# Optimization experiments

Measured on AMD Instinct MI355X. Metric: run time of the kernel, lower is better.

## Reference

```python
import jax, jax.numpy as jnp
import numpy as np

N_NODES = 50000
N_EDGES = 600000
IN_DIM = 128
HID = 128
OUT_DIM = 10
N_GRAPHS = 512
LN_EPS = 1e-5
N_CELLS = 4  # len(macro_architecture) + 1


def setup_inputs() -> dict:
    key = jax.random.key(0)
    ks = jax.random.split(key, 8)
    s = 0.05
    x = jax.random.normal(ks[0], (N_NODES, IN_DIM), dtype=jnp.float32)
    edge_index = jax.random.randint(ks[1], (2, N_EDGES), 0, N_NODES, dtype=jnp.int32)
    batch = jnp.sort(jax.random.randint(ks[2], (N_NODES,), 0, N_GRAPHS, dtype=jnp.int32))
    return {
        "x": x,
        "edge_index": edge_index,
        "batch": batch,
        "W_pre": jax.random.normal(ks[3], (IN_DIM, HID), dtype=jnp.float32) * s,
        "b_pre": jnp.zeros((HID,), jnp.float32),
        "conv_W": jax.random.normal(ks[4], (N_CELLS, HID, HID), dtype=jnp.float32) * s,
        "conv_b": jnp.zeros((N_CELLS, HID), jnp.float32),
        "ln_g": jnp.ones((N_CELLS, HID), jnp.float32),
        "ln_b": jnp.zeros((N_CELLS, HID), jnp.float32),
        "W_post": jax.random.normal(ks[5], (HID, OUT_DIM), dtype=jnp.float32) * s,
        "b_post": jnp.zeros((OUT_DIM,), jnp.float32),
    }


def _gcn_conv(x, W, b, src, dst):
    """GCNConv: add self-loops, symmetric deg^-1/2 normalization, gather-scatter."""
    n = x.shape[0]
    h = x @ W                                   # [N, HID]
    loops = jnp.arange(n, dtype=src.dtype)
    s = jnp.concatenate([src, loops])           # [E + N]
    d = jnp.concatenate([dst, loops])
    deg = jax.ops.segment_sum(jnp.ones_like(d, jnp.float32), d, num_segments=n)
    dinv = jax.lax.rsqrt(jnp.maximum(deg, 1.0))  # deg >= 1 via self-loops
    coef = dinv[s] * dinv[d]                    # [E + N]
    out = jax.ops.segment_sum(h[s] * coef[:, None], d, num_segments=n)
    return out + b


def _layer_norm(x, g, b):
    mu = jnp.mean(x, axis=-1, keepdims=True)
    var = jnp.var(x, axis=-1, keepdims=True)
    return (x - mu) * jax.lax.rsqrt(var + LN_EPS) * g + b


def _cell(x, i, conv_W, conv_b, ln_g, ln_b, src, dst):
    h = _gcn_conv(x, conv_W[i], conv_b[i], src, dst)
    return jax.nn.relu(_layer_norm(h, ln_g[i], ln_b[i]))


def reference(x, edge_index, batch, W_pre, b_pre, conv_W, conv_b, ln_g, ln_b, W_post, b_post):
    src, dst = edge_index[0], edge_index[1]
    # pre MLP
    h0 = x @ W_pre + b_pre
    # state node 0 (all 3 outgoing edges active -> identical output reused)
    n0 = _cell(h0, 0, conv_W, conv_b, ln_g, ln_b, src, dst)
    # state node 1: input = node0's output
    n1 = _cell(n0, 1, conv_W, conv_b, ln_g, ln_b, src, dst)
    # second-to-last node: sum of [-2] outputs (n0, n1)
    s2l = _cell(n0 + n1, 2, conv_W, conv_b, ln_g, ln_b, src, dst)
    # last node: sum of [-1] outputs (n0, n1) + second-to-last output
    last = _cell(n0 + n1 + s2l, 3, conv_W, conv_b, ln_g, ln_b, src, dst)
    # sum pooling by graph id, then post MLP
    pooled = jax.ops.segment_sum(last, batch, num_segments=N_GRAPHS)  # [G, HID]
    return pooled @ W_post + b_post
```

## Files before the change

kernel.cpp:

```cpp
#include <hip/hip_runtime.h>

#define HID 128
#define LN_EPS 1e-5f

using f32x2 = __attribute__((ext_vector_type(2))) float;
using f32x4 = __attribute__((ext_vector_type(4))) float;
using s16x8 = __attribute__((ext_vector_type(8))) short;

__device__ inline float bl2f(unsigned u) { u <<= 16; return __builtin_bit_cast(float, u); }
__device__ inline float bh2f(unsigned u) { u &= 0xffff0000u; return __builtin_bit_cast(float, u); }
__device__ inline float sb2f(short s) {
  unsigned u = ((unsigned)(unsigned short)s) << 16;
  return __builtin_bit_cast(float, u);
}
__device__ inline unsigned f2b_bits(float f) {
  unsigned u = __builtin_bit_cast(unsigned, f);
  return (u + 0x7fffu + ((u >> 16) & 1u)) >> 16;
}
__device__ inline short f2b(float f) { return (short)f2b_bits(f); }
__device__ inline unsigned pack2(float a, float b) { return f2b_bits(a) | (f2b_bits(b) << 16); }
__device__ inline f32x2 up2(unsigned u) {
  f32x2 r; r.x = bl2f(u); r.y = bh2f(u); return r;
}


__global__ __launch_bounds__(64) void prep_w_kernel(const float* __restrict__ W_pre,
                                                    const float* __restrict__ conv_W,
                                                    short* __restrict__ Wt) {
  int b = blockIdx.x;
  int w = b >> 7, n = b & 127;
  const float* W = (w == 0) ? W_pre : conv_W + (size_t)(w - 1) * HID * HID;
  int t = threadIdx.x;
  float f0 = W[(2 * t) * HID + n];
  float f1 = W[(2 * t + 1) * HID + n];
  ((unsigned*)Wt)[(size_t)(w * HID + n) * 64 + t] = pack2(f0, f1);
}


__global__ void zero_ints_kernel(int* __restrict__ p, int n) {
  int i = blockIdx.x * blockDim.x + threadIdx.x;
  if (i < n) p[i] = 0;
}

__global__ void deg_count_kernel(const int* __restrict__ dst, int E, int* __restrict__ deg) {
  int e = blockIdx.x * blockDim.x + threadIdx.x;
  if (e < E) atomicAdd(&deg[dst[e]], 1);
}

__global__ __launch_bounds__(256) void alloc_kernel(const int* __restrict__ deg,
                                                    int* __restrict__ start,
                                                    int* __restrict__ cur,
                                                    float* __restrict__ dinv,
                                                    int* __restrict__ cnt, int n) {
  __shared__ int wt[4];
  __shared__ int bbase;
  int t = threadIdx.x, lane = t & 63, wid = t >> 6;
  int i = blockIdx.x * 256 + t;
  int d = (i < n) ? deg[i] : 0;
  int x = d;
  #pragma unroll
  for (int off = 1; off < 64; off <<= 1) {
    int u = __shfl_up(x, off, 64);
    if (lane >= off) x += u;
  }
  if (lane == 63) wt[wid] = x;
  __syncthreads();
  if (t == 0) bbase = atomicAdd(cnt, wt[0] + wt[1] + wt[2] + wt[3]);
  __syncthreads();
  int wbase = bbase;
  for (int w = 0; w < wid; ++w) wbase += wt[w];
  int excl = wbase + x - d;
  if (i < n) {
    start[i] = excl;
    cur[i] = excl;
    dinv[i] = rsqrtf((float)(d + 1));
  }
}

__global__ void fill_csr_kernel(const int* __restrict__ src, const int* __restrict__ dst,
                                int E, int* __restrict__ cur, int* __restrict__ col) {
  int e = blockIdx.x * blockDim.x + threadIdx.x;
  if (e < E) {
    int d = dst[e];
    int p = atomicAdd(&cur[d], 1);
    col[p] = src[e];
  }
}

#define HNODES 4096
__global__ __launch_bounds__(256) void hist_kernel(const int* __restrict__ deg,
                                                   int* __restrict__ hist, int n) {
  __shared__ int lh[64];
  int t = threadIdx.x;
  if (t < 64) lh[t] = 0;
  __syncthreads();
  int nend = min(n, (int)(blockIdx.x + 1) * HNODES);
  for (int i = blockIdx.x * HNODES + t; i < nend; i += 256)
    atomicAdd(&lh[min(deg[i], 63)], 1);
  __syncthreads();
  if (t < 64 && lh[t]) atomicAdd(&hist[t * 16], lh[t]);
}

__global__ __launch_bounds__(64) void binoff_kernel(const int* __restrict__ hist,
                                                    int* __restrict__ bincur) {
  int lane = threadIdx.x;
  int rb = 63 - lane;
  int v = hist[rb * 16];
  int x = v;
  #pragma unroll
  for (int off = 1; off < 64; off <<= 1) {
    int u = __shfl_up(x, off, 64);
    if (lane >= off) x += u;
  }
  bincur[rb * 16] = x - v;
}

#define SNODES 1024
__global__ __launch_bounds__(256) void scatter_kernel(const int* __restrict__ deg,
                                                      int* __restrict__ bincur,
                                                      int* __restrict__ perm, int n) {
  __shared__ int lh[64];
  __shared__ int lbase[64];
  int t = threadIdx.x;
  if (t < 64) lh[t] = 0;
  __syncthreads();
  int nstart = blockIdx.x * SNODES;
  int nend = min(n, nstart + SNODES);
  int myb[4], myrank[4];
  int cnt = 0;
  for (int i = nstart + t; i < nend; i += 256) {
    int b = min(deg[i], 63);
    myb[cnt] = b;
    myrank[cnt] = atomicAdd(&lh[b], 1);
    ++cnt;
  }
  __syncthreads();
  if (t < 64) lbase[t] = lh[t] ? atomicAdd(&bincur[t * 16], lh[t]) : 0;
  __syncthreads();
  int k = 0;
  for (int i = nstart + t; i < nend; i += 256, ++k)
    perm[lbase[myb[k]] + myrank[k]] = i;
}


__global__ __launch_bounds__(256) void gemm_mfma_kernel(
    const float* __restrict__ Xf, const short* __restrict__ Wt,
    const float* __restrict__ bias, const float* __restrict__ dinv,
    short* __restrict__ Y, int M) {
  __shared__ short lds[4 * 32 * HID];
  int t = threadIdx.x;
  int wave = t >> 6, l = t & 63;
  int lg = l >> 4, lr = l & 15;
  int mb = blockIdx.x * 128 + wave * 32;

  const f32x4 z4 = {0.f, 0.f, 0.f, 0.f};
  f32x4 acc[2][8];
  #pragma unroll
  for (int i = 0; i < 2; ++i)
    #pragma unroll
    for (int j = 0; j < 8; ++j) acc[i][j] = z4;

  #pragma unroll
  for (int kk = 0; kk < 4; ++kk) {
    int k0 = kk * 32 + lg * 8;
    s16x8 a[2];
    #pragma unroll
    for (int mf = 0; mf < 2; ++mf) {
      int row = mb + mf * 16 + lr;
      s16x8 av = {0, 0, 0, 0, 0, 0, 0, 0};
      if (row < M) {
        const float4* p = (const float4*)(Xf + (size_t)row * HID + k0);
        float4 x0 = p[0], x1 = p[1];
        av[0] = f2b(x0.x); av[1] = f2b(x0.y); av[2] = f2b(x0.z); av[3] = f2b(x0.w);
        av[4] = f2b(x1.x); av[5] = f2b(x1.y); av[6] = f2b(x1.z); av[7] = f2b(x1.w);
      }
      a[mf] = av;
    }
    #pragma unroll
    for (int nf = 0; nf < 8; ++nf) {
      s16x8 b = *(const s16x8*)(Wt + (size_t)(nf * 16 + lr) * HID + k0);
      acc[0][nf] = __builtin_amdgcn_mfma_f32_16x16x32_bf16(a[0], b, acc[0][nf], 0, 0, 0);
      acc[1][nf] = __builtin_amdgcn_mfma_f32_16x16x32_bf16(a[1], b, acc[1][nf], 0, 0, 0);
    }
  }

  float bv[8];
  #pragma unroll
  for (int nf = 0; nf < 8; ++nf) bv[nf] = bias[nf * 16 + lr];

  short* wsl = lds + wave * 32 * HID;
  #pragma unroll
  for (int mf = 0; mf < 2; ++mf) {
    #pragma unroll
    for (int r = 0; r < 4; ++r) {
      int ri = mf * 16 + lg * 4 + r;
      int row = mb + ri;
      float dv = (row < M) ? dinv[row] : 1.f;
      #pragma unroll
      for (int nf = 0; nf < 8; ++nf) {
        float v = (acc[mf][nf][r] + bv[nf]) * dv;
        wsl[ri * HID + nf * 16 + lr] = f2b(v);
      }
    }
  }
  __syncthreads();

  #pragma unroll
  for (int it = 0; it < 8; ++it) {
    int ro = it * 4 + lg;
    int row = mb + ro;
    s16x8 v = *(const s16x8*)(wsl + it * 512 + l * 8);
    if (row < M) *(s16x8*)(Y + (size_t)row * HID + lr * 8) = v;
  }
}


__global__ __launch_bounds__(256, 8) void cell_kernel(
    const short* __restrict__ Sin, const int* __restrict__ start,
    const int* __restrict__ deg, const float* __restrict__ dinv,
    const int* __restrict__ col, const int* __restrict__ perm,
    const short* __restrict__ Wt, const float* __restrict__ bconv,
    const float* __restrict__ lng, const float* __restrict__ lnb,
    short* __restrict__ Sout, int N, int mode) {
  __shared__ short Zs[16 * HID];
  __shared__ float red[16][4][2];
  int t = threadIdx.x;
  int wave = t >> 6, l = t & 63, lr = l & 15, sub = l >> 4;
  const uint4* GR = (const uint4*)Sin;

  int rowL = wave * 4 + sub;
  int slot = blockIdx.x * 16 + rowL;
  int v = (slot < N) ? perm[slot] : -1;
  int zofs = rowL * HID + ((lr * 8) ^ ((rowL & 7) << 3));
  if (v >= 0) {
    uint4 us = GR[(size_t)v * 16 + lr];
    f32x2 a0 = up2(us.x), a1 = up2(us.y), a2 = up2(us.z), a3 = up2(us.w);
    int lo = start[v], hi = lo + deg[v];
    int j = lo;
    for (; j + 4 <= hi; j += 4) {
      int c0 = col[j], c1 = col[j + 1], c2 = col[j + 2], c3 = col[j + 3];
      uint4 u0 = GR[(size_t)c0 * 16 + lr];
      uint4 u1 = GR[(size_t)c1 * 16 + lr];
      uint4 u2 = GR[(size_t)c2 * 16 + lr];
      uint4 u3 = GR[(size_t)c3 * 16 + lr];
      a0 += up2(u0.x) + up2(u1.x);  a1 += up2(u0.y) + up2(u1.y);
      a2 += up2(u0.z) + up2(u1.z);  a3 += up2(u0.w) + up2(u1.w);
      a0 += up2(u2.x) + up2(u3.x);  a1 += up2(u2.y) + up2(u3.y);
      a2 += up2(u2.z) + up2(u3.z);  a3 += up2(u2.w) + up2(u3.w);
    }
    for (; j < hi; ++j) {
      uint4 u0 = GR[(size_t)col[j] * 16 + lr];
      a0 += up2(u0.x); a1 += up2(u0.y); a2 += up2(u0.z); a3 += up2(u0.w);
    }
    float d = dinv[v];
    uint4 q;
    q.x = pack2(a0.x * d, a0.y * d);
    q.y = pack2(a1.x * d, a1.y * d);
    q.z = pack2(a2.x * d, a2.y * d);
    q.w = pack2(a3.x * d, a3.y * d);
    *(uint4*)&Zs[zofs] = q;
  } else {
    *(uint4*)&Zs[zofs] = make_uint4(0u, 0u, 0u, 0u);
  }
  __syncthreads();

  f32x4 acc0 = {0.f, 0.f, 0.f, 0.f}, acc1 = {0.f, 0.f, 0.f, 0.f};
  int base = wave * 32;
  #pragma unroll
  for (int kk = 0; kk < 4; ++kk) {
    int k0 = kk * 32 + sub * 8;
    s16x8 af = *(const s16x8*)&Zs[lr * HID + (k0 ^ ((lr & 7) << 3))];
    s16x8 bf0 = *(const s16x8*)(Wt + (size_t)(base + lr) * HID + k0);
    s16x8 bf1 = *(const s16x8*)(Wt + (size_t)(base + 16 + lr) * HID + k0);
    acc0 = __builtin_amdgcn_mfma_f32_16x16x32_bf16(af, bf0, acc0, 0, 0, 0);
    acc1 = __builtin_amdgcn_mfma_f32_16x16x32_bf16(af, bf1, acc1, 0, 0, 0);
  }
  int c0 = base + lr, c1 = base + 16 + lr;
  float bc0 = bconv[c0], bc1 = bconv[c1];
  float h0[4], h1[4], s1[4], s2[4];
  #pragma unroll
  for (int r = 0; r < 4; ++r) {
    h0[r] = acc0[r] + bc0;
    h1[r] = acc1[r] + bc1;
    s1[r] = h0[r] + h1[r];
    s2[r] = h0[r] * h0[r] + h1[r] * h1[r];
  }
  #pragma unroll
  for (int off = 1; off <= 8; off <<= 1) {
    #pragma unroll
    for (int r = 0; r < 4; ++r) {
      s1[r] += __shfl_xor(s1[r], off, 64);
      s2[r] += __shfl_xor(s2[r], off, 64);
    }
  }
  if (lr == 0) {
    #pragma unroll
    for (int r = 0; r < 4; ++r) {
      red[sub * 4 + r][wave][0] = s1[r];
      red[sub * 4 + r][wave][1] = s2[r];
    }
  }
  __syncthreads();
  float gl0 = lng[c0], bl0 = lnb[c0], gl1 = lng[c1], bl1 = lnb[c1];
  #pragma unroll
  for (int r = 0; r < 4; ++r) {
    int row = sub * 4 + r;
    const float4* rp = (const float4*)&red[row][0][0];
    float4 v0 = rp[0], v1 = rp[1];
    float t1 = v0.x + v0.z + v1.x + v1.z;
    float t2 = v0.y + v0.w + v1.y + v1.w;
    float mu = t1 * (1.f / HID);
    float var = t2 * (1.f / HID) - mu * mu;
    float inv = rsqrtf(fmaxf(var, 0.f) + LN_EPS);
    float yv0 = fmaxf(fmaf((h0[r] - mu) * inv, gl0, bl0), 0.f);
    float yv1 = fmaxf(fmaf((h1[r] - mu) * inv, gl1, bl1), 0.f);
    int sw = (row & 7) << 3;
    Zs[row * HID + (c0 ^ sw)] = f2b(yv0);
    Zs[row * HID + (c1 ^ sw)] = f2b(yv1);
  }
  __syncthreads();

  {
    int row = t >> 4, qq = t & 15;
    int slot2 = blockIdx.x * 16 + row;
    if (slot2 < N) {
      int v2 = perm[slot2];
      s16x8 y8 = *(const s16x8*)&Zs[row * HID + ((qq * 8) ^ ((row & 7) << 3))];
      float yv[8];
      #pragma unroll
      for (int i = 0; i < 8; ++i) yv[i] = sb2f(y8[i]);
      uint4 o;
      if (mode == 2) {
        o.x = pack2(yv[0], yv[1]); o.y = pack2(yv[2], yv[3]);
        o.z = pack2(yv[4], yv[5]); o.w = pack2(yv[6], yv[7]);
      } else if (mode == 0) {
        float d = dinv[v2];
        o.x = pack2(yv[0] * d, yv[1] * d); o.y = pack2(yv[2] * d, yv[3] * d);
        o.z = pack2(yv[4] * d, yv[5] * d); o.w = pack2(yv[6] * d, yv[7] * d);
      } else {
        float d = dinv[v2];
        uint4 ui = GR[(size_t)v2 * 16 + qq];
        o.x = pack2(bl2f(ui.x) + yv[0] * d, bh2f(ui.x) + yv[1] * d);
        o.y = pack2(bl2f(ui.y) + yv[2] * d, bh2f(ui.y) + yv[3] * d);
        o.z = pack2(bl2f(ui.z) + yv[4] * d, bh2f(ui.z) + yv[5] * d);
        o.w = pack2(bl2f(ui.w) + yv[6] * d, bh2f(ui.w) + yv[7] * d);
      }
      ((uint4*)Sout)[(size_t)v2 * 16 + qq] = o;
    }
  }
}


__device__ inline int lower_bound_i(const int* a, int n, int key) {
  int lo = 0, hi = n;
  while (lo < hi) { int m = (lo + hi) >> 1; if (a[m] < key) lo = m + 1; else hi = m; }
  return lo;
}

__global__ __launch_bounds__(128) void pool_post_kernel(
    const short* __restrict__ Yl, const int* __restrict__ batch, int n,
    const float* __restrict__ Wp, const float* __restrict__ bp,
    float* __restrict__ out, int n_out) {
  int g = blockIdx.x, t = threadIdx.x;
  int wave = t >> 6;
  int lr = t & 15, slot = t >> 4;
  int lo = lower_bound_i(batch, n, g);
  int hi = lower_bound_i(batch, n, g + 1);
  const uint4* YR = (const uint4*)Yl;
  float a[8] = {0.f, 0.f, 0.f, 0.f, 0.f, 0.f, 0.f, 0.f};
  for (int r = lo + slot; r < hi; r += 8) {
    uint4 u = YR[(size_t)r * 16 + lr];
    a[0] += bl2f(u.x); a[1] += bh2f(u.x);
    a[2] += bl2f(u.y); a[3] += bh2f(u.y);
    a[4] += bl2f(u.z); a[5] += bh2f(u.z);
    a[6] += bl2f(u.w); a[7] += bh2f(u.w);
  }
  #pragma unroll
  for (int i = 0; i < 8; ++i) {
    a[i] += __shfl_xor(a[i], 16, 64);
    a[i] += __shfl_xor(a[i], 32, 64);
  }
  __shared__ float ls[2][HID];
  if ((slot & 3) == 0) {
    #pragma unroll
    for (int i = 0; i < 8; ++i) ls[wave][8 * lr + i] = a[i];
  }
  __syncthreads();
  if (t < n_out) {
    float o = bp[t];
    #pragma unroll 8
    for (int k = 0; k < HID; ++k) o = fmaf(ls[0][k] + ls[1][k], Wp[k * n_out + t], o);
    out[g * n_out + t] = o;
  }
}


extern "C" void kernel_launch(void* const* d_in, const int* in_sizes, int n_in,
                              void* d_out, int out_size, void* d_ws, size_t ws_size,
                              hipStream_t stream) {
  const float* x      = (const float*)d_in[0];
  const int*   ei     = (const int*)d_in[1];
  const int*   batch  = (const int*)d_in[2];
  const float* W_pre  = (const float*)d_in[3];
  const float* b_pre  = (const float*)d_in[4];
  const float* conv_W = (const float*)d_in[5];
  const float* conv_b = (const float*)d_in[6];
  const float* ln_g   = (const float*)d_in[7];
  const float* ln_b   = (const float*)d_in[8];
  const float* W_post = (const float*)d_in[9];
  const float* b_post = (const float*)d_in[10];
  float* out = (float*)d_out;

  const int N = in_sizes[2];
  const int E = in_sizes[1] / 2;
  const int OUT_DIM = 10;
  const int NG = out_size / OUT_DIM;

  char* p = (char*)d_ws;
  short* SA  = (short*)p;            p += (size_t)N * HID * 2;
  short* SB  = (short*)p;            p += (size_t)N * HID * 2;
  short* Wt  = (short*)p;            p += (size_t)5 * HID * HID * 2;
  float* dinv = (float*)p;           p += (size_t)N * 4;
  int* deg   = (int*)p;              p += (size_t)(N + 1) * 4;
  int* startv = (int*)p;             p += (size_t)N * 4;
  int* cur   = (int*)p;              p += (size_t)N * 4;
  int* col   = (int*)p;              p += (size_t)E * 4;
  int* perm  = (int*)p;              p += (size_t)N * 4;
  int* hist  = (int*)p;              p += 64 * 16 * 4;
  int* bincur = (int*)p;             p += 64 * 16 * 4;
  int* cnt   = deg + N;

  const int* srcp = ei;
  const int* dstp = ei + E;

  int nb256 = (N + 255) / 256;
  int eb256 = (E + 255) / 256;
  int gemm_grid = (N + 127) / 128;
  int cell_grid = (N + 15) / 16;
  int hist_grid = (N + HNODES - 1) / HNODES;
  int scat_grid = (N + SNODES - 1) / SNODES;

  prep_w_kernel<<<5 * HID, 64, 0, stream>>>(W_pre, conv_W, Wt);

  zero_ints_kernel<<<nb256, 256, 0, stream>>>(deg, N + 1);
  zero_ints_kernel<<<4, 256, 0, stream>>>(hist, 64 * 16);
  deg_count_kernel<<<eb256, 256, 0, stream>>>(dstp, E, deg);
  alloc_kernel<<<nb256, 256, 0, stream>>>(deg, startv, cur, dinv, cnt, N);
  fill_csr_kernel<<<eb256, 256, 0, stream>>>(srcp, dstp, E, cur, col);
  hist_kernel<<<hist_grid, 256, 0, stream>>>(deg, hist, N);
  binoff_kernel<<<1, 64, 0, stream>>>(hist, bincur);
  scatter_kernel<<<scat_grid, 256, 0, stream>>>(deg, bincur, perm, N);

  gemm_mfma_kernel<<<gemm_grid, 256, 0, stream>>>(x, Wt + 0 * 16384, b_pre, dinv, SA, N);

  cell_kernel<<<cell_grid, 256, 0, stream>>>(SA, startv, deg, dinv, col, perm, Wt + 1 * 16384,
                                             conv_b + 0 * HID, ln_g + 0 * HID, ln_b + 0 * HID,
                                             SB, N, 0);
  cell_kernel<<<cell_grid, 256, 0, stream>>>(SB, startv, deg, dinv, col, perm, Wt + 2 * 16384,
                                             conv_b + 1 * HID, ln_g + 1 * HID, ln_b + 1 * HID,
                                             SA, N, 1);
  cell_kernel<<<cell_grid, 256, 0, stream>>>(SA, startv, deg, dinv, col, perm, Wt + 3 * 16384,
                                             conv_b + 2 * HID, ln_g + 2 * HID, ln_b + 2 * HID,
                                             SB, N, 1);
  cell_kernel<<<cell_grid, 256, 0, stream>>>(SB, startv, deg, dinv, col, perm, Wt + 4 * 16384,
                                             conv_b + 3 * HID, ln_g + 3 * HID, ln_b + 3 * HID,
                                             SA, N, 2);

  pool_post_kernel<<<NG, 128, 0, stream>>>(SA, batch, N, W_post, b_post, out, OUT_DIM);
}
```

Baseline: 269.6 us.

## Use persistent cell kernel with atomic chunk counter; fold histogram into alloc

The cell kernel becomes persistent: a fixed grid of 2048 blocks pulls 16-node chunks from a global atomic counter, one counter per cell. This is meant to cut block launch and scheduling overhead and balance work across nodes of uneven degree. The degree histogram now accumulates inside alloc_kernel, removing hist_kernel. Zeroing is merged into a single launch over one contiguous region holding deg, counters and hist. The cost is an extra atomic and barrier per chunk.

```diff
diff --git a/kernel.cpp b/kernel.cpp
--- a/kernel.cpp
+++ b/kernel.cpp
@@ -51,10 +51,13 @@
                                                     int* __restrict__ start,
                                                     int* __restrict__ cur,
                                                     float* __restrict__ dinv,
-                                                    int* __restrict__ cnt, int n) {
+                                                    int* __restrict__ cnt,
+                                                    int* __restrict__ hist, int n) {
   __shared__ int wt[4];
   __shared__ int bbase;
+  __shared__ int lh[64];
   int t = threadIdx.x, lane = t & 63, wid = t >> 6;
+  if (t < 64) lh[t] = 0;
   int i = blockIdx.x * 256 + t;
   int d = (i < n) ? deg[i] : 0;
   int x = d;
@@ -65,6 +68,7 @@
   }
   if (lane == 63) wt[wid] = x;
   __syncthreads();
+  if (i < n) atomicAdd(&lh[min(d, 63)], 1);
   if (t == 0) bbase = atomicAdd(cnt, wt[0] + wt[1] + wt[2] + wt[3]);
   __syncthreads();
   int wbase = bbase;
@@ -75,6 +79,7 @@
     cur[i] = excl;
     dinv[i] = rsqrtf((float)(d + 1));
   }
+  if (t < 64 && lh[t]) atomicAdd(&hist[t * 16], lh[t]);
 }
 
 __global__ void fill_csr_kernel(const int* __restrict__ src, const int* __restrict__ dst,
@@ -85,20 +90,6 @@
     int p = atomicAdd(&cur[d], 1);
     col[p] = src[e];
   }
-}
-
-#define HNODES 4096
-__global__ __launch_bounds__(256) void hist_kernel(const int* __restrict__ deg,
-                                                   int* __restrict__ hist, int n) {
-  __shared__ int lh[64];
-  int t = threadIdx.x;
-  if (t < 64) lh[t] = 0;
-  __syncthreads();
-  int nend = min(n, (int)(blockIdx.x + 1) * HNODES);
-  for (int i = blockIdx.x * HNODES + t; i < nend; i += 256)
-    atomicAdd(&lh[min(deg[i], 63)], 1);
-  __syncthreads();
-  if (t < 64 && lh[t]) atomicAdd(&hist[t * 16], lh[t]);
 }
 
 __global__ __launch_bounds__(64) void binoff_kernel(const int* __restrict__ hist,
@@ -221,132 +212,142 @@
     const int* __restrict__ col, const int* __restrict__ perm,
     const short* __restrict__ Wt, const float* __restrict__ bconv,
     const float* __restrict__ lng, const float* __restrict__ lnb,
-    short* __restrict__ Sout, int N, int mode) {
+    short* __restrict__ Sout, int* __restrict__ ctr, int N, int mode) {
   __shared__ short Zs[16 * HID];
   __shared__ float red[16][4][2];
+  __shared__ int s_chunk;
   int t = threadIdx.x;
   int wave = t >> 6, l = t & 63, lr = l & 15, sub = l >> 4;
   const uint4* GR = (const uint4*)Sin;
-
-  int rowL = wave * 4 + sub;
-  int slot = blockIdx.x * 16 + rowL;
-  int v = (slot < N) ? perm[slot] : -1;
-  int zofs = rowL * HID + ((lr * 8) ^ ((rowL & 7) << 3));
-  if (v >= 0) {
-    uint4 us = GR[(size_t)v * 16 + lr];
-    f32x2 a0 = up2(us.x), a1 = up2(us.y), a2 = up2(us.z), a3 = up2(us.w);
-    int lo = start[v], hi = lo + deg[v];
-    int j = lo;
-    for (; j + 4 <= hi; j += 4) {
-      int c0 = col[j], c1 = col[j + 1], c2 = col[j + 2], c3 = col[j + 3];
-      uint4 u0 = GR[(size_t)c0 * 16 + lr];
-      uint4 u1 = GR[(size_t)c1 * 16 + lr];
-      uint4 u2 = GR[(size_t)c2 * 16 + lr];
-      uint4 u3 = GR[(size_t)c3 * 16 + lr];
-      a0 += up2(u0.x) + up2(u1.x);  a1 += up2(u0.y) + up2(u1.y);
-      a2 += up2(u0.z) + up2(u1.z);  a3 += up2(u0.w) + up2(u1.w);
-      a0 += up2(u2.x) + up2(u3.x);  a1 += up2(u2.y) + up2(u3.y);
-      a2 += up2(u2.z) + up2(u3.z);  a3 += up2(u2.w) + up2(u3.w);
-    }
-    for (; j < hi; ++j) {
-      uint4 u0 = GR[(size_t)col[j] * 16 + lr];
-      a0 += up2(u0.x); a1 += up2(u0.y); a2 += up2(u0.z); a3 += up2(u0.w);
-    }
-    float d = dinv[v];
-    uint4 q;
-    q.x = pack2(a0.x * d, a0.y * d);
-    q.y = pack2(a1.x * d, a1.y * d);
-    q.z = pack2(a2.x * d, a2.y * d);
-    q.w = pack2(a3.x * d, a3.y * d);
-    *(uint4*)&Zs[zofs] = q;
-  } else {
-    *(uint4*)&Zs[zofs] = make_uint4(0u, 0u, 0u, 0u);
-  }
-  __syncthreads();
-
-  f32x4 acc0 = {0.f, 0.f, 0.f, 0.f}, acc1 = {0.f, 0.f, 0.f, 0.f};
-  int base = wave * 32;
-  #pragma unroll
-  for (int kk = 0; kk < 4; ++kk) {
-    int k0 = kk * 32 + sub * 8;
-    s16x8 af = *(const s16x8*)&Zs[lr * HID + (k0 ^ ((lr & 7) << 3))];
-    s16x8 bf0 = *(const s16x8*)(Wt + (size_t)(base + lr) * HID + k0);
-    s16x8 bf1 = *(const s16x8*)(Wt + (size_t)(base + 16 + lr) * HID + k0);
-    acc0 = __builtin_amdgcn_mfma_f32_16x16x32_bf16(af, bf0, acc0, 0, 0, 0);
-    acc1 = __builtin_amdgcn_mfma_f32_16x16x32_bf16(af, bf1, acc1, 0, 0, 0);
-  }
-  int c0 = base + lr, c1 = base + 16 + lr;
-  float bc0 = bconv[c0], bc1 = bconv[c1];
-  float h0[4], h1[4], s1[4], s2[4];
-  #pragma unroll
-  for (int r = 0; r < 4; ++r) {
-    h0[r] = acc0[r] + bc0;
-    h1[r] = acc1[r] + bc1;
-    s1[r] = h0[r] + h1[r];
-    s2[r] = h0[r] * h0[r] + h1[r] * h1[r];
-  }
-  #pragma unroll
-  for (int off = 1; off <= 8; off <<= 1) {
+  int nchunks = (N + 15) >> 4;
+
+  while (true) {
+    if (t == 0) s_chunk = atomicAdd(ctr, 1);
+    __syncthreads();
+    int chunk = s_chunk;
+    if (chunk >= nchunks) break;
+
+    int rowL = wave * 4 + sub;
+    int slot = chunk * 16 + rowL;
+    int v = (slot < N) ? perm[slot] : -1;
+    int zofs = rowL * HID + ((lr * 8) ^ ((rowL & 7) << 3));
+    if (v >= 0) {
+      uint4 us = GR[(size_t)v * 16 + lr];
+      f32x2 a0 = up2(us.x), a1 = up2(us.y), a2 = up2(us.z), a3 = up2(us.w);
+      int lo = start[v], hi = lo + deg[v];
+      int j = lo;
+      for (; j + 4 <= hi; j += 4) {
+        int c0 = col[j], c1 = col[j + 1], c2 = col[j + 2], c3 = col[j + 3];
+        uint4 u0 = GR[(size_t)c0 * 16 + lr];
+        uint4 u1 = GR[(size_t)c1 * 16 + lr];
+        uint4 u2 = GR[(size_t)c2 * 16 + lr];
+        uint4 u3 = GR[(size_t)c3 * 16 + lr];
+        a0 += up2(u0.x) + up2(u1.x);  a1 += up2(u0.y) + up2(u1.y);
+        a2 += up2(u0.z) + up2(u1.z);  a3 += up2(u0.w) + up2(u1.w);
+        a0 += up2(u2.x) + up2(u3.x);  a1 += up2(u2.y) + up2(u3.y);
+        a2 += up2(u2.z) + up2(u3.z);  a3 += up2(u2.w) + up2(u3.w);
+      }
+      for (; j < hi; ++j) {
+        uint4 u0 = GR[(size_t)col[j] * 16 + lr];
+        a0 += up2(u0.x); a1 += up2(u0.y); a2 += up2(u0.z); a3 += up2(u0.w);
+      }
+      float d = dinv[v];
+      uint4 q;
+      q.x = pack2(a0.x * d, a0.y * d);
+      q.y = pack2(a1.x * d, a1.y * d);
+      q.z = pack2(a2.x * d, a2.y * d);
+      q.w = pack2(a3.x * d, a3.y * d);
+      *(uint4*)&Zs[zofs] = q;
+    } else {
+      *(uint4*)&Zs[zofs] = make_uint4(0u, 0u, 0u, 0u);
+    }
+    __syncthreads();
+
+    f32x4 acc0 = {0.f, 0.f, 0.f, 0.f}, acc1 = {0.f, 0.f, 0.f, 0.f};
+    int base = wave * 32;
+    #pragma unroll
+    for (int kk = 0; kk < 4; ++kk) {
+      int k0 = kk * 32 + sub * 8;
+      s16x8 af = *(const s16x8*)&Zs[lr * HID + (k0 ^ ((lr & 7) << 3))];
+      s16x8 bf0 = *(const s16x8*)(Wt + (size_t)(base + lr) * HID + k0);
+      s16x8 bf1 = *(const s16x8*)(Wt + (size_t)(base + 16 + lr) * HID + k0);
+      acc0 = __builtin_amdgcn_mfma_f32_16x16x32_bf16(af, bf0, acc0, 0, 0, 0);
+      acc1 = __builtin_amdgcn_mfma_f32_16x16x32_bf16(af, bf1, acc1, 0, 0, 0);
+    }
+    int c0 = base + lr, c1 = base + 16 + lr;
+    float bc0 = bconv[c0], bc1 = bconv[c1];
+    float h0[4], h1[4], s1[4], s2[4];
     #pragma unroll
     for (int r = 0; r < 4; ++r) {
-      s1[r] += __shfl_xor(s1[r], off, 64);
-      s2[r] += __shfl_xor(s2[r], off, 64);
-    }
-  }
-  if (lr == 0) {
+      h0[r] = acc0[r] + bc0;
+      h1[r] = acc1[r] + bc1;
+      s1[r] = h0[r] + h1[r];
+      s2[r] = h0[r] * h0[r] + h1[r] * h1[r];
+    }
+    #pragma unroll
+    for (int off = 1; off <= 8; off <<= 1) {
+      #pragma unroll
+      for (int r = 0; r < 4; ++r) {
+        s1[r] += __shfl_xor(s1[r], off, 64);
+        s2[r] += __shfl_xor(s2[r], off, 64);
+      }
+    }
+    if (lr == 0) {
+      #pragma unroll
+      for (int r = 0; r < 4; ++r) {
+        red[sub * 4 + r][wave][0] = s1[r];
+        red[sub * 4 + r][wave][1] = s2[r];
+      }
+    }
+    __syncthreads();
+    float gl0 = lng[c0], bl0 = lnb[c0], gl1 = lng[c1], bl1 = lnb[c1];
     #pragma unroll
     for (int r = 0; r < 4; ++r) {
-      red[sub * 4 + r][wave][0] = s1[r];
-      red[sub * 4 + r][wave][1] = s2[r];
-    }
-  }
-  __syncthreads();
-  float gl0 = lng[c0], bl0 = lnb[c0], gl1 = lng[c1], bl1 = lnb[c1];
-  #pragma unroll
-  for (int r = 0; r < 4; ++r) {
-    int row = sub * 4 + r;
-    const float4* rp = (const float4*)&red[row][0][0];
-    float4 v0 = rp[0], v1 = rp[1];
-    float t1 = v0.x + v0.z + v1.x + v1.z;
-    float t2 = v0.y + v0.w + v1.y + v1.w;
-    float mu = t1 * (1.f / HID);
-    float var = t2 * (1.f / HID) - mu * mu;
-    float inv = rsqrtf(fmaxf(var, 0.f) + LN_EPS);
-    float yv0 = fmaxf(fmaf((h0[r] - mu) * inv, gl0, bl0), 0.f);
-    float yv1 = fmaxf(fmaf((h1[r] - mu) * inv, gl1, bl1), 0.f);
-    int sw = (row & 7) << 3;
-    Zs[row * HID + (c0 ^ sw)] = f2b(yv0);
-    Zs[row * HID + (c1 ^ sw)] = f2b(yv1);
-  }
-  __syncthreads();
-
-  {
-    int row = t >> 4, qq = t & 15;
-    int slot2 = blockIdx.x * 16 + row;
-    if (slot2 < N) {
-      int v2 = perm[slot2];
-      s16x8 y8 = *(const s16x8*)&Zs[row * HID + ((qq * 8) ^ ((row & 7) << 3))];
-      float yv[8];
-      #pragma unroll
-      for (int i = 0; i < 8; ++i) yv[i] = sb2f(y8[i]);
-      uint4 o;
-      if (mode == 2) {
-        o.x = pack2(yv[0], yv[1]); o.y = pack2(yv[2], yv[3]);
-        o.z = pack2(yv[4], yv[5]); o.w = pack2(yv[6], yv[7]);
-      } else if (mode == 0) {
-        float d = dinv[v2];
-        o.x = pack2(yv[0] * d, yv[1] * d); o.y = pack2(yv[2] * d, yv[3] * d);
-        o.z = pack2(yv[4] * d, yv[5] * d); o.w = pack2(yv[6] * d, yv[7] * d);
-      } else {
-        float d = dinv[v2];
-        uint4 ui = GR[(size_t)v2 * 16 + qq];
-        o.x = pack2(bl2f(ui.x) + yv[0] * d, bh2f(ui.x) + yv[1] * d);
-        o.y = pack2(bl2f(ui.y) + yv[2] * d, bh2f(ui.y) + yv[3] * d);
-        o.z = pack2(bl2f(ui.z) + yv[4] * d, bh2f(ui.z) + yv[5] * d);
-        o.w = pack2(bl2f(ui.w) + yv[6] * d, bh2f(ui.w) + yv[7] * d);
-      }
-      ((uint4*)Sout)[(size_t)v2 * 16 + qq] = o;
-    }
+      int row = sub * 4 + r;
+      const float4* rp = (const float4*)&red[row][0][0];
+      float4 v0 = rp[0], v1 = rp[1];
+      float t1 = v0.x + v0.z + v1.x + v1.z;
+      float t2 = v0.y + v0.w + v1.y + v1.w;
+      float mu = t1 * (1.f / HID);
+      float var = t2 * (1.f / HID) - mu * mu;
+      float inv = rsqrtf(fmaxf(var, 0.f) + LN_EPS);
+      float yv0 = fmaxf(fmaf((h0[r] - mu) * inv, gl0, bl0), 0.f);
+      float yv1 = fmaxf(fmaf((h1[r] - mu) * inv, gl1, bl1), 0.f);
+      int sw = (row & 7) << 3;
+      Zs[row * HID + (c0 ^ sw)] = f2b(yv0);
+      Zs[row * HID + (c1 ^ sw)] = f2b(yv1);
+    }
+    __syncthreads();
+
+    {
+      int row = t >> 4, qq = t & 15;
+      int slot2 = chunk * 16 + row;
+      if (slot2 < N) {
+        int v2 = perm[slot2];
+        s16x8 y8 = *(const s16x8*)&Zs[row * HID + ((qq * 8) ^ ((row & 7) << 3))];
+        float yv[8];
+        #pragma unroll
+        for (int i = 0; i < 8; ++i) yv[i] = sb2f(y8[i]);
+        uint4 o;
+        if (mode == 2) {
+          o.x = pack2(yv[0], yv[1]); o.y = pack2(yv[2], yv[3]);
+          o.z = pack2(yv[4], yv[5]); o.w = pack2(yv[6], yv[7]);
+        } else if (mode == 0) {
+          float d = dinv[v2];
+          o.x = pack2(yv[0] * d, yv[1] * d); o.y = pack2(yv[2] * d, yv[3] * d);
+          o.z = pack2(yv[4] * d, yv[5] * d); o.w = pack2(yv[6] * d, yv[7] * d);
+        } else {
+          float d = dinv[v2];
+          uint4 ui = GR[(size_t)v2 * 16 + qq];
+          o.x = pack2(bl2f(ui.x) + yv[0] * d, bh2f(ui.x) + yv[1] * d);
+          o.y = pack2(bl2f(ui.y) + yv[2] * d, bh2f(ui.y) + yv[3] * d);
+          o.z = pack2(bl2f(ui.z) + yv[4] * d, bh2f(ui.z) + yv[5] * d);
+          o.w = pack2(bl2f(ui.w) + yv[6] * d, bh2f(ui.w) + yv[7] * d);
+        }
+        ((uint4*)Sout)[(size_t)v2 * 16 + qq] = o;
+      }
+    }
+    __syncthreads();
   }
 }
 
@@ -421,33 +422,32 @@
   short* SB  = (short*)p;            p += (size_t)N * HID * 2;
   short* Wt  = (short*)p;            p += (size_t)5 * HID * HID * 2;
   float* dinv = (float*)p;           p += (size_t)N * 4;
-  int* deg   = (int*)p;              p += (size_t)(N + 1) * 4;
+  int* deg   = (int*)p;              p += (size_t)(N + 8 + 64 * 16) * 4;
+  int* cnt   = deg + N;
+  int* ctrs  = deg + N + 1;
+  int* hist  = deg + N + 8;
   int* startv = (int*)p;             p += (size_t)N * 4;
   int* cur   = (int*)p;              p += (size_t)N * 4;
   int* col   = (int*)p;              p += (size_t)E * 4;
   int* perm  = (int*)p;              p += (size_t)N * 4;
-  int* hist  = (int*)p;              p += 64 * 16 * 4;
   int* bincur = (int*)p;             p += 64 * 16 * 4;
-  int* cnt   = deg + N;
 
   const int* srcp = ei;
   const int* dstp = ei + E;
 
+  int zero_n = N + 8 + 64 * 16;
   int nb256 = (N + 255) / 256;
   int eb256 = (E + 255) / 256;
   int gemm_grid = (N + 127) / 128;
-  int cell_grid = (N + 15) / 16;
-  int hist_grid = (N + HNODES - 1) / HNODES;
+  int cell_grid = 2048;
   int scat_grid = (N + SNODES - 1) / SNODES;
 
   prep_w_kernel<<<5 * HID, 64, 0, stream>>>(W_pre, conv_W, Wt);
 
-  zero_ints_kernel<<<nb256, 256, 0, stream>>>(deg, N + 1);
-  zero_ints_kernel<<<4, 256, 0, stream>>>(hist, 64 * 16);
+  zero_ints_kernel<<<(zero_n + 255) / 256, 256, 0, stream>>>(deg, zero_n);
   deg_count_kernel<<<eb256, 256, 0, stream>>>(dstp, E, deg);
-  alloc_kernel<<<nb256, 256, 0, stream>>>(deg, startv, cur, dinv, cnt, N);
+  alloc_kernel<<<nb256, 256, 0, stream>>>(deg, startv, cur, dinv, cnt, hist, N);
   fill_csr_kernel<<<eb256, 256, 0, stream>>>(srcp, dstp, E, cur, col);
-  hist_kernel<<<hist_grid, 256, 0, stream>>>(deg, hist, N);
   binoff_kernel<<<1, 64, 0, stream>>>(hist, bincur);
   scatter_kernel<<<scat_grid, 256, 0, stream>>>(deg, bincur, perm, N);
 
@@ -455,16 +455,16 @@
 
   cell_kernel<<<cell_grid, 256, 0, stream>>>(SA, startv, deg, dinv, col, perm, Wt + 1 * 16384,
                                              conv_b + 0 * HID, ln_g + 0 * HID, ln_b + 0 * HID,
-                                             SB, N, 0);
+                                             SB, ctrs + 0, N, 0);
   cell_kernel<<<cell_grid, 256, 0, stream>>>(SB, startv, deg, dinv, col, perm, Wt + 2 * 16384,
                                              conv_b + 1 * HID, ln_g + 1 * HID, ln_b + 1 * HID,
-                                             SA, N, 1);
+                                             SA, ctrs + 1, N, 1);
   cell_kernel<<<cell_grid, 256, 0, stream>>>(SA, startv, deg, dinv, col, perm, Wt + 3 * 16384,
                                              conv_b + 2 * HID, ln_g + 2 * HID, ln_b + 2 * HID,
-                                             SB, N, 1);
+                                             SB, ctrs + 2, N, 1);
   cell_kernel<<<cell_grid, 256, 0, stream>>>(SB, startv, deg, dinv, col, perm, Wt + 4 * 16384,
                                              conv_b + 3 * HID, ln_g + 3 * HID, ln_b + 3 * HID,
-                                             SA, N, 2);
+                                             SA, ctrs + 3, N, 2);
 
   pool_post_kernel<<<NG, 128, 0, stream>>>(SA, batch, N, W_post, b_post, out, OUT_DIM);
 }
```

After: 451.5 us. +67.5%, slower.
